# Kernel optimization log

Hardware: AMD Instinct MI355X
Metric: run time of the kernel (lower is better)

Reference implementation:

```python
import jax, jax.numpy as jnp
import numpy as np

# levels for the auction iterations: j = 7..-1 gives level = -4^j, j = -2 gives level = 0
_LEVEL_JS = list(range(7, -3, -1))


def approx_match(xyz1, xyz2):
    # xyz1: [B,N,3], xyz2: [B,M,3] -> soft match matrix [B,N,M]
    B, N, _ = xyz1.shape
    M = xyz2.shape[1]
    multiL = 1.0 if N >= M else float(M // N)
    multiR = float(N // M) if N >= M else 1.0
    # pairwise squared distances [B,N,M]
    d2 = jnp.sum((xyz1[:, :, None, :] - xyz2[:, None, :, :]) ** 2, axis=-1)
    levels = jnp.array([0.0 if j == -2 else -(4.0 ** j) for j in _LEVEL_JS],
                       dtype=xyz1.dtype)

    def step(carry, level):
        match, remainL, remainR = carry
        w = jnp.exp(level * d2) * remainR[:, None, :]                      # [B,N,M]
        # row-normalize to each left point's remaining mass
        w = w * (remainL / (jnp.sum(w, axis=2) + 1e-9))[:, :, None]
        # clip columns to right points' remaining capacity
        ss = jnp.sum(w, axis=1) + 1e-9                                     # [B,M]
        w = w * jnp.minimum(remainR / ss, 1.0)[:, None, :]
        match = match + w
        remainL = jnp.maximum(remainL - jnp.sum(w, axis=2), 0.0)
        remainR = jnp.maximum(remainR - jnp.sum(w, axis=1), 0.0)
        return (match, remainL, remainR), None

    init = (jnp.zeros_like(d2),
            jnp.full((B, N), multiL, dtype=d2.dtype),
            jnp.full((B, M), multiR, dtype=d2.dtype))
    (match, _, _), _ = jax.lax.scan(step, init, levels)
    return match


def match_cost(xyz1, xyz2, match):
    # cost[b] = sum_{k,l} match[b,k,l] * ||xyz1[b,k] - xyz2[b,l]||
    d = jnp.sqrt(jnp.sum((xyz1[:, :, None, :] - xyz2[:, None, :, :]) ** 2, axis=-1))
    return jnp.sum(match * d, axis=(1, 2))


def setup_inputs() -> dict:
    key = jax.random.key(0)
    k1, k2 = jax.random.split(key)
    B, N, M = 8, 2048, 2048
    input1 = jax.random.normal(k1, (B, N, 3), dtype=jnp.float32)
    input2 = jax.random.normal(k2, (B, M, 3), dtype=jnp.float32)
    return {"input1": input1, "input2": input2}


def reference(input1, input2):
    match = approx_match(input1, input2)
    return match_cost(input1, input2, match)
```

## Files before the change

kernel.cpp:

```cpp
#include <hip/hip_runtime.h>
#include <hip/hip_fp16.h>


#define BATCH 8
#define NPTS 2048
#define MPTS 2048
#define BLOCK 256
#define ROWS 16
#define LOG2E 1.44269504088896340736f

__device__ __forceinline__ float fast_exp2(float x) {
  return __builtin_amdgcn_exp2f(x);
}

__device__ __forceinline__ float fast_sqrt(float a) {
  return __builtin_amdgcn_sqrtf(a);
}

__device__ __forceinline__ float packh2(float c, float r) {
  __half2 h = __halves2half2(__float2half_rn(c), __float2half_rn(r));
  return __builtin_bit_cast(float, h);
}

__device__ __forceinline__ void load8(const float4* q, int r0, float k,
                                      float* x, float* y, float* z) {
  int b4 = (r0 >> 2) * 3;
  float4 q0 = q[b4], q1 = q[b4 + 1], q2 = q[b4 + 2];
  float4 q3 = q[b4 + 3], q4 = q[b4 + 4], q5 = q[b4 + 5];
  x[0] = k * q0.x; y[0] = k * q0.y; z[0] = k * q0.z;
  x[1] = k * q0.w; y[1] = k * q1.x; z[1] = k * q1.y;
  x[2] = k * q1.z; y[2] = k * q1.w; z[2] = k * q2.x;
  x[3] = k * q2.y; y[3] = k * q2.z; z[3] = k * q2.w;
  x[4] = k * q3.x; y[4] = k * q3.y; z[4] = k * q3.z;
  x[5] = k * q3.w; y[5] = k * q4.x; z[5] = k * q4.y;
  x[6] = k * q4.z; y[6] = k * q4.w; z[6] = k * q5.x;
  x[7] = k * q5.y; y[7] = k * q5.z; z[7] = k * q5.w;
}

__global__ __launch_bounds__(BLOCK, 4) void emd_A0_kernel(
    const float* __restrict__ xyz1, const float* __restrict__ xyz2,
    float* __restrict__ rowscale, float* __restrict__ out,
    float* __restrict__ t1buf, float k0) {
  __shared__ float4 sP[MPTS];
  __shared__ float sRed[ROWS * 4];

  const int tid = threadIdx.x;
  const int bid = blockIdx.x;
  const int b = bid >> 7;
  const int t0 = (bid & 127) * ROWS;
  if (bid == 0 && tid < BATCH) { out[tid] = 0.0f; t1buf[tid] = 0.0f; }

  const float4* q2 = (const float4*)(xyz2 + (size_t)b * MPTS * 3);
  for (int g = tid; g < MPTS / 4; g += BLOCK) {
    float4 a = q2[3 * g], bb = q2[3 * g + 1], c = q2[3 * g + 2];
    sP[4 * g + 0] = make_float4(k0 * a.x, k0 * a.y, k0 * a.z, 0.0f);
    sP[4 * g + 1] = make_float4(k0 * a.w, k0 * bb.x, k0 * bb.y, 0.0f);
    sP[4 * g + 2] = make_float4(k0 * bb.z, k0 * bb.w, k0 * c.x, 0.0f);
    sP[4 * g + 3] = make_float4(k0 * c.y, k0 * c.z, k0 * c.w, 0.0f);
  }
  __syncthreads();

  const int wave = tid >> 6, lane = tid & 63;
  const int phase = lane >> 1, rg = lane & 1;
  const int r0 = t0 + rg * 8;
  float x1[8], y1[8], z1[8], acc[8];
  load8((const float4*)(xyz1 + (size_t)b * NPTS * 3), r0, k0, x1, y1, z1);
#pragma unroll
  for (int j = 0; j < 8; ++j) acc[j] = 0.0f;
  const int mb = wave * 512 + phase;
#pragma unroll 2
  for (int it = 0; it < 16; ++it) {
    float4 v = sP[mb + it * 32];
#pragma unroll
    for (int j = 0; j < 8; ++j) {
      float dx = x1[j] - v.x, dy = y1[j] - v.y, dz = z1[j] - v.z;
      float s = __builtin_fmaf(dx, dx, __builtin_fmaf(dy, dy, dz * dz));
      acc[j] += fast_exp2(-s);
    }
  }
#pragma unroll
  for (int j = 0; j < 8; ++j) {
    acc[j] += __shfl_xor(acc[j], 2, 64);
    acc[j] += __shfl_xor(acc[j], 4, 64);
    acc[j] += __shfl_xor(acc[j], 8, 64);
    acc[j] += __shfl_xor(acc[j], 16, 64);
    acc[j] += __shfl_xor(acc[j], 32, 64);
  }
  if (lane < 2) {
#pragma unroll
    for (int j = 0; j < 8; ++j) sRed[(rg * 8 + j) * 4 + wave] = acc[j];
  }
  __syncthreads();
  if (tid < ROWS) {
    float s = sRed[tid * 4] + sRed[tid * 4 + 1] + sRed[tid * 4 + 2] +
              sRed[tid * 4 + 3];
    rowscale[(size_t)b * NPTS + t0 + tid] = 1.0f / (s + 1e-9f);
  }
}

template <bool FIRST>
__global__ __launch_bounds__(BLOCK, 4) void emd_B_kernel(
    const float* __restrict__ xyz1, const float* __restrict__ xyz2,
    const float* __restrict__ rowscale, float* __restrict__ remainR,
    float* __restrict__ colcoef, float k) {
  __shared__ float4 sP[NPTS];
  __shared__ float sRed[ROWS * 4];

  const int tid = threadIdx.x;
  const int bid = blockIdx.x;
  const int b = bid >> 7;
  const int t0 = (bid & 127) * ROWS;

  const float4* q1 = (const float4*)(xyz1 + (size_t)b * NPTS * 3);
  const float4* w4 = (const float4*)(rowscale + (size_t)b * NPTS);
  for (int g = tid; g < NPTS / 4; g += BLOCK) {
    float4 a = q1[3 * g], bb = q1[3 * g + 1], c = q1[3 * g + 2];
    float4 w = w4[g];
    sP[4 * g + 0] = make_float4(k * a.x, k * a.y, k * a.z, w.x);
    sP[4 * g + 1] = make_float4(k * a.w, k * bb.x, k * bb.y, w.y);
    sP[4 * g + 2] = make_float4(k * bb.z, k * bb.w, k * c.x, w.z);
    sP[4 * g + 3] = make_float4(k * c.y, k * c.z, k * c.w, w.w);
  }
  __syncthreads();

  const int wave = tid >> 6, lane = tid & 63;
  const int phase = lane >> 1, rg = lane & 1;
  const int c0 = t0 + rg * 8;
  float x2[8], y2[8], z2[8], acc[8];
  load8((const float4*)(xyz2 + (size_t)b * MPTS * 3), c0, k, x2, y2, z2);
#pragma unroll
  for (int j = 0; j < 8; ++j) acc[j] = 0.0f;
  const int nb = wave * 512 + phase;
#pragma unroll 2
  for (int it = 0; it < 16; ++it) {
    float4 v = sP[nb + it * 32];
#pragma unroll
    for (int j = 0; j < 8; ++j) {
      float dx = x2[j] - v.x, dy = y2[j] - v.y, dz = z2[j] - v.z;
      float s = __builtin_fmaf(dx, dx, __builtin_fmaf(dy, dy, dz * dz));
      acc[j] = __builtin_fmaf(fast_exp2(-s), v.w, acc[j]);
    }
  }
#pragma unroll
  for (int j = 0; j < 8; ++j) {
    acc[j] += __shfl_xor(acc[j], 2, 64);
    acc[j] += __shfl_xor(acc[j], 4, 64);
    acc[j] += __shfl_xor(acc[j], 8, 64);
    acc[j] += __shfl_xor(acc[j], 16, 64);
    acc[j] += __shfl_xor(acc[j], 32, 64);
  }
  if (lane < 2) {
#pragma unroll
    for (int j = 0; j < 8; ++j) sRed[(rg * 8 + j) * 4 + wave] = acc[j];
  }
  __syncthreads();
  if (tid < ROWS) {
    float t1 = sRed[tid * 4] + sRed[tid * 4 + 1] + sRed[tid * 4 + 2] +
               sRed[tid * 4 + 3];
    size_t idx = (size_t)b * MPTS + t0 + tid;
    float rr = FIRST ? 1.0f : remainR[idx];
    float colsum = rr * t1;
    float cs = fminf(rr / (colsum + 1e-9f), 1.0f);
    colcoef[idx] = rr * cs;
    remainR[idx] = fmaxf(rr - colsum * cs, 0.0f);
  }
}

template <bool FIRST, bool LAST>
__global__ __launch_bounds__(BLOCK, 4) void emd_CA_kernel(
    const float* __restrict__ xyz1, const float* __restrict__ xyz2,
    float* __restrict__ rowscale, float* __restrict__ remainL,
    const float* __restrict__ remainR, const float* __restrict__ colcoef,
    float* __restrict__ out, float* __restrict__ t1buf, float kS, float invK) {
  __shared__ float4 sP[MPTS];
  __shared__ float sRedS[ROWS * 4];
  __shared__ float sRedC[ROWS * 4];
  __shared__ float sRedR[ROWS * 4];
  __shared__ float sCost[ROWS];
  __shared__ float sRs[ROWS];

  const int tid = threadIdx.x;
  const int bid = blockIdx.x;
  const int b = bid >> 7;
  const int t0 = (bid & 127) * ROWS;

  const float4* q2 = (const float4*)(xyz2 + (size_t)b * MPTS * 3);
  const float4* cc4 = (const float4*)(colcoef + (size_t)b * MPTS);
  const float4* rr4 = (const float4*)(remainR + (size_t)b * MPTS);
  for (int g = tid; g < MPTS / 4; g += BLOCK) {
    float4 a = q2[3 * g], bb = q2[3 * g + 1], c = q2[3 * g + 2];
    float4 cc = cc4[g], rr = rr4[g];
    sP[4 * g + 0] = make_float4(kS * a.x, kS * a.y, kS * a.z, packh2(cc.x, rr.x));
    sP[4 * g + 1] = make_float4(kS * a.w, kS * bb.x, kS * bb.y, packh2(cc.y, rr.y));
    sP[4 * g + 2] = make_float4(kS * bb.z, kS * bb.w, kS * c.x, packh2(cc.z, rr.z));
    sP[4 * g + 3] = make_float4(kS * c.y, kS * c.z, kS * c.w, packh2(cc.w, rr.w));
  }
  __syncthreads();

  const int wave = tid >> 6, lane = tid & 63;
  const int phase = lane >> 2, rg = lane & 3;
  const int r0 = t0 + rg * 4;
  float x1[4], y1[4], z1[4];
  {
    const float4* q1 = (const float4*)(xyz1 + (size_t)b * NPTS * 3);
    int b4 = (r0 >> 2) * 3;
    float4 a = q1[b4], bb = q1[b4 + 1], c = q1[b4 + 2];
    x1[0] = kS * a.x;  y1[0] = kS * a.y;  z1[0] = kS * a.z;
    x1[1] = kS * a.w;  y1[1] = kS * bb.x; z1[1] = kS * bb.y;
    x1[2] = kS * bb.z; y1[2] = kS * bb.w; z1[2] = kS * c.x;
    x1[3] = kS * c.y;  y1[3] = kS * c.z;  z1[3] = kS * c.w;
  }
  float accS[4] = {0.f, 0.f, 0.f, 0.f};
  float accC[4] = {0.f, 0.f, 0.f, 0.f};
  float accR[4] = {0.f, 0.f, 0.f, 0.f};
  const int mb = wave * 512 + phase;
#pragma unroll 4
  for (int it = 0; it < 32; ++it) {
    float4 v = sP[mb + it * 16];
    __half2 h = __builtin_bit_cast(__half2, v.w);
    float cc = __low2float(h);
    float rr = __high2float(h);
#pragma unroll
    for (int j = 0; j < 4; ++j) {
      float dx = x1[j] - v.x, dy = y1[j] - v.y, dz = z1[j] - v.z;
      float s = __builtin_fmaf(dx, dx, __builtin_fmaf(dy, dy, dz * dz));
      float sq = fast_sqrt(s);
      float e1, e2;
      if (LAST) {
        e2 = 1.0f;
        e1 = fast_exp2(-s);
      } else {
        e2 = fast_exp2(-s);
        float e2s = e2 * e2;
        e1 = e2s * e2s;
      }
      float t = e1 * cc;
      accS[j] += t;
      accC[j] = __builtin_fmaf(t, sq, accC[j]);
      if (LAST) accR[j] += rr;
      else      accR[j] = __builtin_fmaf(e2, rr, accR[j]);
    }
  }
#pragma unroll
  for (int j = 0; j < 4; ++j) {
    accS[j] += __shfl_xor(accS[j], 4, 64);
    accS[j] += __shfl_xor(accS[j], 8, 64);
    accS[j] += __shfl_xor(accS[j], 16, 64);
    accS[j] += __shfl_xor(accS[j], 32, 64);
    accC[j] += __shfl_xor(accC[j], 4, 64);
    accC[j] += __shfl_xor(accC[j], 8, 64);
    accC[j] += __shfl_xor(accC[j], 16, 64);
    accC[j] += __shfl_xor(accC[j], 32, 64);
    accR[j] += __shfl_xor(accR[j], 4, 64);
    accR[j] += __shfl_xor(accR[j], 8, 64);
    accR[j] += __shfl_xor(accR[j], 16, 64);
    accR[j] += __shfl_xor(accR[j], 32, 64);
  }
  if (lane < 4) {
#pragma unroll
    for (int j = 0; j < 4; ++j) {
      sRedS[(rg * 4 + j) * 4 + wave] = accS[j];
      sRedC[(rg * 4 + j) * 4 + wave] = accC[j];
      sRedR[(rg * 4 + j) * 4 + wave] = accR[j];
    }
  }
  __syncthreads();
  if (tid < ROWS) {
    float S2 = sRedS[tid * 4] + sRedS[tid * 4 + 1] + sRedS[tid * 4 + 2] +
               sRedS[tid * 4 + 3];
    float C = sRedC[tid * 4] + sRedC[tid * 4 + 1] + sRedC[tid * 4 + 2] +
              sRedC[tid * 4 + 3];
    float R = sRedR[tid * 4] + sRedR[tid * 4 + 1] + sRedR[tid * 4 + 2] +
              sRedR[tid * 4 + 3];
    size_t idx = (size_t)b * NPTS + t0 + tid;
    float rs = rowscale[idx];
    float rl = FIRST ? 1.0f : remainL[idx];
    float rlN = fmaxf(rl - rs * S2, 0.0f);
    remainL[idx] = rlN;
    float rsN = rlN / (R + 1e-9f);
    rowscale[idx] = rsN;
    sCost[tid] = rs * C * invK;
    if (LAST) sRs[tid] = rsN;
  }
  __syncthreads();
  if (tid == 0) {
    float t = 0.0f;
#pragma unroll
    for (int i = 0; i < ROWS; ++i) t += sCost[i];
    atomicAdd(out + b, t);
    if (LAST) {
      float r = 0.0f;
#pragma unroll
      for (int i = 0; i < ROWS; ++i) r += sRs[i];
      atomicAdd(t1buf + b, r);
    }
  }
}

__global__ __launch_bounds__(BLOCK, 4) void emd_C9_kernel(
    const float* __restrict__ xyz1, const float* __restrict__ xyz2,
    const float* __restrict__ rowscale, const float* __restrict__ remainR,
    const float* __restrict__ t1buf, float* __restrict__ out) {
  __shared__ float4 sP[MPTS];
  __shared__ float sRed[ROWS * 4];
  __shared__ float sCost[ROWS];

  const int tid = threadIdx.x;
  const int bid = blockIdx.x;
  const int b = bid >> 7;
  const int t0 = (bid & 127) * ROWS;
  const int wave = tid >> 6, lane = tid & 63;
  const float t1 = t1buf[b];

  const float4* q2 = (const float4*)(xyz2 + (size_t)b * MPTS * 3);
  const float4* rr4 = (const float4*)(remainR + (size_t)b * MPTS);
  for (int g = tid; g < MPTS / 4; g += BLOCK) {
    float4 a = q2[3 * g], bb = q2[3 * g + 1], c = q2[3 * g + 2];
    float4 rr = rr4[g];
    float w0 = rr.x * fminf(rr.x / (rr.x * t1 + 1e-9f), 1.0f);
    float w1 = rr.y * fminf(rr.y / (rr.y * t1 + 1e-9f), 1.0f);
    float w2 = rr.z * fminf(rr.z / (rr.z * t1 + 1e-9f), 1.0f);
    float w3 = rr.w * fminf(rr.w / (rr.w * t1 + 1e-9f), 1.0f);
    sP[4 * g + 0] = make_float4(a.x, a.y, a.z, w0);
    sP[4 * g + 1] = make_float4(a.w, bb.x, bb.y, w1);
    sP[4 * g + 2] = make_float4(bb.z, bb.w, c.x, w2);
    sP[4 * g + 3] = make_float4(c.y, c.z, c.w, w3);
  }
  __syncthreads();

  const int phase = lane >> 1, rg = lane & 1;
  const int r0 = t0 + rg * 8;
  float x1[8], y1[8], z1[8], acc[8];
  load8((const float4*)(xyz1 + (size_t)b * NPTS * 3), r0, 1.0f, x1, y1, z1);
#pragma unroll
  for (int j = 0; j < 8; ++j) acc[j] = 0.0f;
  const int mb = wave * 512 + phase;
#pragma unroll 2
  for (int it = 0; it < 16; ++it) {
    float4 v = sP[mb + it * 32];
#pragma unroll
    for (int j = 0; j < 8; ++j) {
      float dx = x1[j] - v.x, dy = y1[j] - v.y, dz = z1[j] - v.z;
      float d2 = __builtin_fmaf(dx, dx, __builtin_fmaf(dy, dy, dz * dz));
      acc[j] = __builtin_fmaf(fast_sqrt(d2), v.w, acc[j]);
    }
  }
#pragma unroll
  for (int j = 0; j < 8; ++j) {
    acc[j] += __shfl_xor(acc[j], 2, 64);
    acc[j] += __shfl_xor(acc[j], 4, 64);
    acc[j] += __shfl_xor(acc[j], 8, 64);
    acc[j] += __shfl_xor(acc[j], 16, 64);
    acc[j] += __shfl_xor(acc[j], 32, 64);
  }
  if (lane < 2) {
#pragma unroll
    for (int j = 0; j < 8; ++j) sRed[(rg * 8 + j) * 4 + wave] = acc[j];
  }
  __syncthreads();
  if (tid < ROWS) {
    float C = sRed[tid * 4] + sRed[tid * 4 + 1] + sRed[tid * 4 + 2] +
              sRed[tid * 4 + 3];
    sCost[tid] = rowscale[(size_t)b * NPTS + t0 + tid] * C;
  }
  __syncthreads();
  if (tid == 0) {
    float t = 0.0f;
#pragma unroll
    for (int i = 0; i < ROWS; ++i) t += sCost[i];
    atomicAdd(out + b, t);
  }
}

extern "C" void kernel_launch(void* const* d_in, const int* in_sizes, int n_in,
                              void* d_out, int out_size, void* d_ws, size_t ws_size,
                              hipStream_t stream) {
  const float* xyz1 = (const float*)d_in[0];
  const float* xyz2 = (const float*)d_in[1];
  float* out = (float*)d_out;
  float* ws = (float*)d_ws;

  float* remainL  = ws;
  float* remainR  = ws + BATCH * NPTS;
  float* rowscale = ws + BATCH * NPTS + BATCH * MPTS;
  float* colcoef  = ws + 2 * BATCH * NPTS + BATCH * MPTS;
  float* t1buf    = ws + 3 * BATCH * NPTS + BATCH * MPTS;

  const float levels[9] = {-16384.f, -4096.f, -1024.f, -256.f, -64.f,
                           -16.f,    -4.f,    -1.f,    -0.25f};
  dim3 grid(BATCH * (NPTS / ROWS));

  emd_A0_kernel<<<grid, BLOCK, 0, stream>>>(
      xyz1, xyz2, rowscale, out, t1buf, sqrtf(-levels[0] * LOG2E));

  for (int l = 0; l < 9; ++l) {
    float kB = sqrtf(-levels[l] * LOG2E);
    float kA = 0.5f * kB;
    if (l == 0) {
      emd_B_kernel<true><<<grid, BLOCK, 0, stream>>>(xyz1, xyz2, rowscale,
                                                     remainR, colcoef, kB);
      emd_CA_kernel<true, false><<<grid, BLOCK, 0, stream>>>(
          xyz1, xyz2, rowscale, remainL, remainR, colcoef, out, t1buf,
          kA, 1.0f / kA);
    } else if (l < 8) {
      emd_B_kernel<false><<<grid, BLOCK, 0, stream>>>(xyz1, xyz2, rowscale,
                                                      remainR, colcoef, kB);
      emd_CA_kernel<false, false><<<grid, BLOCK, 0, stream>>>(
          xyz1, xyz2, rowscale, remainL, remainR, colcoef, out, t1buf,
          kA, 1.0f / kA);
    } else {
      emd_B_kernel<false><<<grid, BLOCK, 0, stream>>>(xyz1, xyz2, rowscale,
                                                      remainR, colcoef, kB);
      emd_CA_kernel<false, true><<<grid, BLOCK, 0, stream>>>(
          xyz1, xyz2, rowscale, remainL, remainR, colcoef, out, t1buf,
          kB, 1.0f / kB);
    }
  }
  emd_C9_kernel<<<grid, BLOCK, 0, stream>>>(xyz1, xyz2, rowscale, remainR,
                                            t1buf, out);
}
```

Before: 368.2 us.

## Fuse column-sum pass into row kernels via atomic scatter, dropping B kernel

Result: faster. 357.4 us (-2.9%).

```diff
diff --git a/kernel.cpp b/kernel.cpp
--- a/kernel.cpp
+++ b/kernel.cpp
@@ -12,11 +12,9 @@
 __device__ __forceinline__ float fast_exp2(float x) {
   return __builtin_amdgcn_exp2f(x);
 }
-
 __device__ __forceinline__ float fast_sqrt(float a) {
   return __builtin_amdgcn_sqrtf(a);
 }
-
 __device__ __forceinline__ float packh2(float c, float r) {
   __half2 h = __halves2half2(__float2half_rn(c), __float2half_rn(r));
   return __builtin_bit_cast(float, h);
@@ -40,23 +38,28 @@
 __global__ __launch_bounds__(BLOCK, 4) void emd_A0_kernel(
     const float* __restrict__ xyz1, const float* __restrict__ xyz2,
     float* __restrict__ rowscale, float* __restrict__ out,
-    float* __restrict__ t1buf, float k0) {
+    float* __restrict__ t9, float* __restrict__ t1acc,
+    float* __restrict__ t1zero, float k0) {
   __shared__ float4 sP[MPTS];
   __shared__ float sRed[ROWS * 4];
+  __shared__ float sRs[ROWS];
 
   const int tid = threadIdx.x;
   const int bid = blockIdx.x;
   const int b = bid >> 7;
   const int t0 = (bid & 127) * ROWS;
-  if (bid == 0 && tid < BATCH) { out[tid] = 0.0f; t1buf[tid] = 0.0f; }
+  const bool desig = (bid & 127) == 0;
+  if (bid == 0 && tid < BATCH) { out[tid] = 0.0f; t9[tid] = 0.0f; }
 
   const float4* q2 = (const float4*)(xyz2 + (size_t)b * MPTS * 3);
+  float4* z4 = (float4*)(t1zero + (size_t)b * MPTS);
   for (int g = tid; g < MPTS / 4; g += BLOCK) {
     float4 a = q2[3 * g], bb = q2[3 * g + 1], c = q2[3 * g + 2];
     sP[4 * g + 0] = make_float4(k0 * a.x, k0 * a.y, k0 * a.z, 0.0f);
     sP[4 * g + 1] = make_float4(k0 * a.w, k0 * bb.x, k0 * bb.y, 0.0f);
     sP[4 * g + 2] = make_float4(k0 * bb.z, k0 * bb.w, k0 * c.x, 0.0f);
     sP[4 * g + 3] = make_float4(k0 * c.y, k0 * c.z, k0 * c.w, 0.0f);
+    if (desig) z4[g] = make_float4(0.f, 0.f, 0.f, 0.f);
   }
   __syncthreads();
 
@@ -94,75 +97,29 @@
   if (tid < ROWS) {
     float s = sRed[tid * 4] + sRed[tid * 4 + 1] + sRed[tid * 4 + 2] +
               sRed[tid * 4 + 3];
-    rowscale[(size_t)b * NPTS + t0 + tid] = 1.0f / (s + 1e-9f);
-  }
-}
-
-template <bool FIRST>
-__global__ __launch_bounds__(BLOCK, 4) void emd_B_kernel(
-    const float* __restrict__ xyz1, const float* __restrict__ xyz2,
-    const float* __restrict__ rowscale, float* __restrict__ remainR,
-    float* __restrict__ colcoef, float k) {
-  __shared__ float4 sP[NPTS];
-  __shared__ float sRed[ROWS * 4];
-
-  const int tid = threadIdx.x;
-  const int bid = blockIdx.x;
-  const int b = bid >> 7;
-  const int t0 = (bid & 127) * ROWS;
-
-  const float4* q1 = (const float4*)(xyz1 + (size_t)b * NPTS * 3);
-  const float4* w4 = (const float4*)(rowscale + (size_t)b * NPTS);
-  for (int g = tid; g < NPTS / 4; g += BLOCK) {
-    float4 a = q1[3 * g], bb = q1[3 * g + 1], c = q1[3 * g + 2];
-    float4 w = w4[g];
-    sP[4 * g + 0] = make_float4(k * a.x, k * a.y, k * a.z, w.x);
-    sP[4 * g + 1] = make_float4(k * a.w, k * bb.x, k * bb.y, w.y);
-    sP[4 * g + 2] = make_float4(k * bb.z, k * bb.w, k * c.x, w.z);
-    sP[4 * g + 3] = make_float4(k * c.y, k * c.z, k * c.w, w.w);
-  }
-  __syncthreads();
-
-  const int wave = tid >> 6, lane = tid & 63;
-  const int phase = lane >> 1, rg = lane & 1;
-  const int c0 = t0 + rg * 8;
-  float x2[8], y2[8], z2[8], acc[8];
-  load8((const float4*)(xyz2 + (size_t)b * MPTS * 3), c0, k, x2, y2, z2);
-#pragma unroll
-  for (int j = 0; j < 8; ++j) acc[j] = 0.0f;
-  const int nb = wave * 512 + phase;
+    float rs = 1.0f / (s + 1e-9f);
+    rowscale[(size_t)b * NPTS + t0 + tid] = rs;
+    sRs[tid] = rs;
+  }
+  __syncthreads();
+
+  float rsn[8];
+#pragma unroll
+  for (int j = 0; j < 8; ++j) rsn[j] = sRs[rg * 8 + j];
+  float* accb = t1acc + (size_t)b * MPTS;
 #pragma unroll 2
   for (int it = 0; it < 16; ++it) {
-    float4 v = sP[nb + it * 32];
+    int idx = mb + it * 32;
+    float4 v = sP[idx];
+    float part = 0.0f;
 #pragma unroll
     for (int j = 0; j < 8; ++j) {
-      float dx = x2[j] - v.x, dy = y2[j] - v.y, dz = z2[j] - v.z;
+      float dx = x1[j] - v.x, dy = y1[j] - v.y, dz = z1[j] - v.z;
       float s = __builtin_fmaf(dx, dx, __builtin_fmaf(dy, dy, dz * dz));
-      acc[j] = __builtin_fmaf(fast_exp2(-s), v.w, acc[j]);
-    }
-  }
-#pragma unroll
-  for (int j = 0; j < 8; ++j) {
-    acc[j] += __shfl_xor(acc[j], 2, 64);
-    acc[j] += __shfl_xor(acc[j], 4, 64);
-    acc[j] += __shfl_xor(acc[j], 8, 64);
-    acc[j] += __shfl_xor(acc[j], 16, 64);
-    acc[j] += __shfl_xor(acc[j], 32, 64);
-  }
-  if (lane < 2) {
-#pragma unroll
-    for (int j = 0; j < 8; ++j) sRed[(rg * 8 + j) * 4 + wave] = acc[j];
-  }
-  __syncthreads();
-  if (tid < ROWS) {
-    float t1 = sRed[tid * 4] + sRed[tid * 4 + 1] + sRed[tid * 4 + 2] +
-               sRed[tid * 4 + 3];
-    size_t idx = (size_t)b * MPTS + t0 + tid;
-    float rr = FIRST ? 1.0f : remainR[idx];
-    float colsum = rr * t1;
-    float cs = fminf(rr / (colsum + 1e-9f), 1.0f);
-    colcoef[idx] = rr * cs;
-    remainR[idx] = fmaxf(rr - colsum * cs, 0.0f);
+      part = __builtin_fmaf(fast_exp2(-s), rsn[j], part);
+    }
+    part += __shfl_xor(part, 1, 64);
+    if (rg == 0) atomicAdd(accb + idx, part);
   }
 }
 
@@ -170,8 +127,10 @@
 __global__ __launch_bounds__(BLOCK, 4) void emd_CA_kernel(
     const float* __restrict__ xyz1, const float* __restrict__ xyz2,
     float* __restrict__ rowscale, float* __restrict__ remainL,
-    const float* __restrict__ remainR, const float* __restrict__ colcoef,
-    float* __restrict__ out, float* __restrict__ t1buf, float kS, float invK) {
+    const float* __restrict__ rrIn, float* __restrict__ rrOut,
+    const float* __restrict__ t1In, float* __restrict__ t1Acc,
+    float* __restrict__ t1Zero, float* __restrict__ out,
+    float* __restrict__ t9, float kS, float invK) {
   __shared__ float4 sP[MPTS];
   __shared__ float sRedS[ROWS * 4];
   __shared__ float sRedC[ROWS * 4];
@@ -183,17 +142,35 @@
   const int bid = blockIdx.x;
   const int b = bid >> 7;
   const int t0 = (bid & 127) * ROWS;
+  const bool desig = (bid & 127) == 0;
 
   const float4* q2 = (const float4*)(xyz2 + (size_t)b * MPTS * 3);
-  const float4* cc4 = (const float4*)(colcoef + (size_t)b * MPTS);
-  const float4* rr4 = (const float4*)(remainR + (size_t)b * MPTS);
+  const float4* rr4 = (const float4*)(rrIn + (size_t)b * MPTS);
+  const float4* t14 = (const float4*)(t1In + (size_t)b * MPTS);
+  float4* ro4 = (float4*)(rrOut + (size_t)b * MPTS);
+  float4* z4 = LAST ? nullptr : (float4*)(t1Zero + (size_t)b * MPTS);
   for (int g = tid; g < MPTS / 4; g += BLOCK) {
     float4 a = q2[3 * g], bb = q2[3 * g + 1], c = q2[3 * g + 2];
-    float4 cc = cc4[g], rr = rr4[g];
-    sP[4 * g + 0] = make_float4(kS * a.x, kS * a.y, kS * a.z, packh2(cc.x, rr.x));
-    sP[4 * g + 1] = make_float4(kS * a.w, kS * bb.x, kS * bb.y, packh2(cc.y, rr.y));
-    sP[4 * g + 2] = make_float4(kS * bb.z, kS * bb.w, kS * c.x, packh2(cc.z, rr.z));
-    sP[4 * g + 3] = make_float4(kS * c.y, kS * c.z, kS * c.w, packh2(cc.w, rr.w));
+    float4 t1v = t14[g];
+    float4 rrv = FIRST ? make_float4(1.f, 1.f, 1.f, 1.f) : rr4[g];
+    float cc[4], rn[4];
+    float rrc[4] = {rrv.x, rrv.y, rrv.z, rrv.w};
+    float t1c[4] = {t1v.x, t1v.y, t1v.z, t1v.w};
+#pragma unroll
+    for (int i = 0; i < 4; ++i) {
+      float colsum = rrc[i] * t1c[i];
+      float cs = fminf(rrc[i] / (colsum + 1e-9f), 1.0f);
+      cc[i] = rrc[i] * cs;
+      rn[i] = fmaxf(rrc[i] - colsum * cs, 0.0f);
+    }
+    sP[4 * g + 0] = make_float4(kS * a.x, kS * a.y, kS * a.z, packh2(cc[0], rn[0]));
+    sP[4 * g + 1] = make_float4(kS * a.w, kS * bb.x, kS * bb.y, packh2(cc[1], rn[1]));
+    sP[4 * g + 2] = make_float4(kS * bb.z, kS * bb.w, kS * c.x, packh2(cc[2], rn[2]));
+    sP[4 * g + 3] = make_float4(kS * c.y, kS * c.z, kS * c.w, packh2(cc[3], rn[3]));
+    if (desig) {
+      ro4[g] = make_float4(rn[0], rn[1], rn[2], rn[3]);
+      if (!LAST) z4[g] = make_float4(0.f, 0.f, 0.f, 0.f);
+    }
   }
   __syncthreads();
 
@@ -280,7 +257,7 @@
     float rsN = rlN / (R + 1e-9f);
     rowscale[idx] = rsN;
     sCost[tid] = rs * C * invK;
-    if (LAST) sRs[tid] = rsN;
+    sRs[tid] = rsN;
   }
   __syncthreads();
   if (tid == 0) {
@@ -292,7 +269,28 @@
       float r = 0.0f;
 #pragma unroll
       for (int i = 0; i < ROWS; ++i) r += sRs[i];
-      atomicAdd(t1buf + b, r);
+      atomicAdd(t9 + b, r);
+    }
+  }
+  if (!LAST) {
+    float rsn[4];
+#pragma unroll
+    for (int j = 0; j < 4; ++j) rsn[j] = sRs[rg * 4 + j];
+    float* accb = t1Acc + (size_t)b * MPTS;
+#pragma unroll 4
+    for (int it = 0; it < 32; ++it) {
+      int idx = mb + it * 16;
+      float4 v = sP[idx];
+      float part = 0.0f;
+#pragma unroll
+      for (int j = 0; j < 4; ++j) {
+        float dx = x1[j] - v.x, dy = y1[j] - v.y, dz = z1[j] - v.z;
+        float s = __builtin_fmaf(dx, dx, __builtin_fmaf(dy, dy, dz * dz));
+        part = __builtin_fmaf(fast_exp2(-s), rsn[j], part);
+      }
+      part += __shfl_xor(part, 1, 64);
+      part += __shfl_xor(part, 2, 64);
+      if (rg == 0) atomicAdd(accb + idx, part);
     }
   }
 }
@@ -300,7 +298,7 @@
 __global__ __launch_bounds__(BLOCK, 4) void emd_C9_kernel(
     const float* __restrict__ xyz1, const float* __restrict__ xyz2,
     const float* __restrict__ rowscale, const float* __restrict__ remainR,
-    const float* __restrict__ t1buf, float* __restrict__ out) {
+    const float* __restrict__ t9, float* __restrict__ out) {
   __shared__ float4 sP[MPTS];
   __shared__ float sRed[ROWS * 4];
   __shared__ float sCost[ROWS];
@@ -310,7 +308,7 @@
   const int b = bid >> 7;
   const int t0 = (bid & 127) * ROWS;
   const int wave = tid >> 6, lane = tid & 63;
-  const float t1 = t1buf[b];
+  const float t1 = t9[b];
 
   const float4* q2 = (const float4*)(xyz2 + (size_t)b * MPTS * 3);
   const float4* rr4 = (const float4*)(remainR + (size_t)b * MPTS);
@@ -380,42 +378,45 @@
   float* out = (float*)d_out;
   float* ws = (float*)d_ws;
 
+  const int BN = BATCH * NPTS, BM = BATCH * MPTS;
   float* remainL  = ws;
-  float* remainR  = ws + BATCH * NPTS;
-  float* rowscale = ws + BATCH * NPTS + BATCH * MPTS;
-  float* colcoef  = ws + 2 * BATCH * NPTS + BATCH * MPTS;
-  float* t1buf    = ws + 3 * BATCH * NPTS + BATCH * MPTS;
+  float* rowscale = ws + BN;
+  float* rrA      = ws + 2 * BN;
+  float* rrB      = ws + 2 * BN + BM;
+  float* t1b      = ws + 2 * BN + 2 * BM;
+  float* t9       = ws + 2 * BN + 5 * BM;
 
   const float levels[9] = {-16384.f, -4096.f, -1024.f, -256.f, -64.f,
                            -16.f,    -4.f,    -1.f,    -0.25f};
   dim3 grid(BATCH * (NPTS / ROWS));
 
+  hipMemsetAsync(t1b, 0, (size_t)BM * sizeof(float), stream);
+
   emd_A0_kernel<<<grid, BLOCK, 0, stream>>>(
-      xyz1, xyz2, rowscale, out, t1buf, sqrtf(-levels[0] * LOG2E));
+      xyz1, xyz2, rowscale, out, t9, t1b , t1b + BM ,
+      sqrtf(-levels[0] * LOG2E));
 
   for (int l = 0; l < 9; ++l) {
     float kB = sqrtf(-levels[l] * LOG2E);
     float kA = 0.5f * kB;
+    float* cur = t1b + (size_t)(l % 3) * BM;
+    float* nxt = t1b + (size_t)((l + 1) % 3) * BM;
+    float* zer = t1b + (size_t)((l + 2) % 3) * BM;
+    float* rin = (l % 2 == 0) ? rrA : rrB;
+    float* rou = (l % 2 == 0) ? rrB : rrA;
     if (l == 0) {
-      emd_B_kernel<true><<<grid, BLOCK, 0, stream>>>(xyz1, xyz2, rowscale,
-                                                     remainR, colcoef, kB);
       emd_CA_kernel<true, false><<<grid, BLOCK, 0, stream>>>(
-          xyz1, xyz2, rowscale, remainL, remainR, colcoef, out, t1buf,
+          xyz1, xyz2, rowscale, remainL, rin, rou, cur, nxt, zer, out, t9,
           kA, 1.0f / kA);
     } else if (l < 8) {
-      emd_B_kernel<false><<<grid, BLOCK, 0, stream>>>(xyz1, xyz2, rowscale,
-                                                      remainR, colcoef, kB);
       emd_CA_kernel<false, false><<<grid, BLOCK, 0, stream>>>(
-          xyz1, xyz2, rowscale, remainL, remainR, colcoef, out, t1buf,
+          xyz1, xyz2, rowscale, remainL, rin, rou, cur, nxt, zer, out, t9,
           kA, 1.0f / kA);
     } else {
-      emd_B_kernel<false><<<grid, BLOCK, 0, stream>>>(xyz1, xyz2, rowscale,
-                                                      remainR, colcoef, kB);
       emd_CA_kernel<false, true><<<grid, BLOCK, 0, stream>>>(
-          xyz1, xyz2, rowscale, remainL, remainR, colcoef, out, t1buf,
+          xyz1, xyz2, rowscale, remainL, rin, rou, cur, nxt, zer, out, t9,
           kB, 1.0f / kB);
     }
   }
-  emd_C9_kernel<<<grid, BLOCK, 0, stream>>>(xyz1, xyz2, rowscale, remainR,
-                                            t1buf, out);
-}
+  emd_C9_kernel<<<grid, BLOCK, 0, stream>>>(xyz1, xyz2, rowscale, rrB, t9, out);
+}
```
